# Performance work log

Measured on AMD Instinct MI355X. Metric: run time of the kernel, lower is better.

## Reference

```python
import jax, jax.numpy as jnp
import numpy as np

B, C, H, W = 8, 256, 64, 64
RED = 8
GAMMA = 1.0

def setup_inputs() -> dict:
    key = jax.random.key(0)
    k0, k1, k2, k3 = jax.random.split(key, 4)
    Cr = C // RED
    scale = 1.0 / np.sqrt(C).astype(np.float32)
    x = jax.random.normal(k0, (B, C, H, W), jnp.float32)
    # 1x1 conv weights (no bias) == channel-mixing matrices [out_c, in_c]
    w1 = jax.random.normal(k1, (Cr, C), jnp.float32) * scale  # query proj
    w2 = jax.random.normal(k2, (Cr, C), jnp.float32) * scale  # key proj
    w3 = jax.random.normal(k3, (C, C), jnp.float32) * scale   # value proj
    return {"x": x, "w1": w1, "w2": w2, "w3": w3}

def reference(x, w1, w2, w3):
    b, c, h, w = x.shape
    n = h * w
    xf = x.reshape(b, c, n)                      # [B,C,N]  (hw_flattern)
    f = jnp.einsum('oc,bcn->bon', w1, xf)        # [B,Cr,N] conv1 (1x1)
    g = jnp.einsum('oc,bcn->bon', w2, xf)        # [B,Cr,N] conv2 (1x1)
    hh = jnp.einsum('oc,bcn->bon', w3, xf)       # [B,C,N]  conv3 (1x1)
    # s = f^T g : [B,N,N]
    s = jnp.einsum('bki,bkj->bij', f, g)
    # NOTE: torch softmax over dim=1 (rows), not the usual last dim
    beta = jax.nn.softmax(s, axis=1)             # [B,N,N]
    o = jnp.einsum('bck,bkn->bcn', hh, beta)     # [B,C,N]
    o = o.reshape(b, c, h, w)
    return GAMMA * o + x
```

## Files before the change

### kernel.cpp

```cpp
#include <hip/hip_runtime.h>
#include <stdint.h>

#define Bsz 8
#define Cc  256
#define Crr 32
#define Nn  4096
#define CN  (Cc * Nn)
#define ITILE 128
#define NIT (Nn / ITILE)

typedef unsigned short u16;
typedef __attribute__((ext_vector_type(8))) short  short8;
typedef __attribute__((ext_vector_type(4))) float  floatx4;
typedef __attribute__((ext_vector_type(4))) unsigned short u16x4;

__device__ __forceinline__ floatx4 mfma16(short8 a, short8 b, floatx4 c) {
  return __builtin_amdgcn_mfma_f32_16x16x32_bf16(a, b, c, 0, 0, 0);
}
__device__ __forceinline__ u16 f2bf(float f) {
  unsigned int u = __builtin_bit_cast(unsigned int, f);
  u = (u + 0x7FFFu + ((u >> 16) & 1u)) >> 16;
  return (u16)u;
}
__device__ __forceinline__ float bf2f(u16 h) {
  unsigned int u = ((unsigned int)h) << 16;
  return __builtin_bit_cast(float, u);
}
__device__ __forceinline__ short8 pack8(const float* __restrict__ p) {
  floatx4 a = *(const floatx4*)p;
  floatx4 b = *(const floatx4*)(p + 4);
  short8 r;
  r[0] = (short)f2bf(a[0]); r[1] = (short)f2bf(a[1]);
  r[2] = (short)f2bf(a[2]); r[3] = (short)f2bf(a[3]);
  r[4] = (short)f2bf(b[0]); r[5] = (short)f2bf(b[1]);
  r[6] = (short)f2bf(b[2]); r[7] = (short)f2bf(b[3]);
  return r;
}
__device__ __forceinline__ void split8(const float* __restrict__ p,
                                       short8& hi, short8& lo) {
  floatx4 a = *(const floatx4*)p;
  floatx4 b = *(const floatx4*)(p + 4);
  float v[8] = {a[0], a[1], a[2], a[3], b[0], b[1], b[2], b[3]};
#pragma unroll
  for (int r = 0; r < 8; ++r) {
    u16 h = f2bf(v[r]);
    hi[r] = (short)h;
    lo[r] = (short)f2bf(v[r] - bf2f(h));
  }
}

template <bool XB16>
__launch_bounds__(256, 2)
__global__ void proj_kernel(const float* __restrict__ x,
                            const float* __restrict__ w1,
                            const float* __restrict__ w2,
                            const float* __restrict__ w3,
                            u16* __restrict__ w3b,
                            u16* __restrict__ fThi, u16* __restrict__ fTlo,
                            u16* __restrict__ gThi, u16* __restrict__ gTlo,
                            u16* __restrict__ xb) {
  const int bid = blockIdx.x;
  const int b   = bid & 7;
  const int nt  = bid >> 3;
  const int tid  = threadIdx.x;
  const int w    = tid >> 6;
  const int lane = tid & 63;
  const int m    = lane & 15;
  const int q    = lane >> 4;
  const int nb0  = nt * 64;
  const int nb   = nb0 + w * 16;

  __shared__ float xs[2][32 * 66];

  const float* xsl = x + (size_t)b * CN;
  const int srow = tid >> 3, scoff = (tid & 7) * 8;

  const floatx4 z4 = {0.f, 0.f, 0.f, 0.f};
  floatx4 aF[2] = {z4, z4}, aG[2] = {z4, z4};

  {
    const float* p = xsl + (size_t)(srow) * Nn + nb0 + scoff;
    floatx4 v0 = *(const floatx4*)p;
    floatx4 v1 = *(const floatx4*)(p + 4);
    float* d = &xs[0][srow * 66 + scoff];
    d[0]=v0[0]; d[1]=v0[1]; d[2]=v0[2]; d[3]=v0[3];
    d[4]=v1[0]; d[5]=v1[1]; d[6]=v1[2]; d[7]=v1[3];
  }

  for (int ci = 0; ci < 8; ++ci) {
    __syncthreads();
    if (ci + 1 < 8) {
      const float* p = xsl + (size_t)((ci + 1) * 32 + srow) * Nn + nb0 + scoff;
      floatx4 v0 = *(const floatx4*)p;
      floatx4 v1 = *(const floatx4*)(p + 4);
      float* d = &xs[(ci + 1) & 1][srow * 66 + scoff];
      d[0]=v0[0]; d[1]=v0[1]; d[2]=v0[2]; d[3]=v0[3];
      d[4]=v1[0]; d[5]=v1[1]; d[6]=v1[2]; d[7]=v1[3];
    }
    const float* xbuf = xs[ci & 1];
    const int c0 = ci * 32;
    short8 xh, xl;
#pragma unroll
    for (int r = 0; r < 8; ++r) {
      float v = xbuf[(q * 8 + r) * 66 + w * 16 + m];
      u16 h = f2bf(v);
      xh[r] = (short)h;
      xl[r] = (short)f2bf(v - bf2f(h));
    }
    if (XB16) {
      const int n  = nb + m;
      const int it = n >> 5;
      const int nq = ((n & 31) >> 3) << 4;
      const int el = n & 7;
      const size_t tb = (size_t)b * CN;
#pragma unroll
      for (int r = 0; r < 8; ++r) {
        int c = c0 + q * 8 + r;
        xb[tb + ((size_t)((it * 16 + (c >> 4)) << 9)) + ((c & 15) + nq) * 8 + el] =
            (u16)xh[r];
      }
    }
#pragma unroll
    for (int ot = 0; ot < 2; ++ot) {
      short8 wh, wl;
      split8(w1 + (size_t)(ot * 16 + m) * Cc + c0 + q * 8, wh, wl);
      aF[ot] = mfma16(xh, wh, aF[ot]);
      aF[ot] = mfma16(xh, wl, aF[ot]);
      aF[ot] = mfma16(xl, wh, aF[ot]);
      split8(w2 + (size_t)(ot * 16 + m) * Cc + c0 + q * 8, wh, wl);
      aG[ot] = mfma16(xh, wh, aG[ot]);
      aG[ot] = mfma16(xh, wl, aG[ot]);
      aG[ot] = mfma16(xl, wh, aG[ot]);
    }
  }

#pragma unroll
  for (int ot = 0; ot < 2; ++ot)
#pragma unroll
    for (int r = 0; r < 4; ++r) {
      int n = nb + q * 4 + r;
      size_t idx = ((size_t)b * Nn + n) * Crr + ot * 16 + m;
      float vf = aF[ot][r];
      u16 hf = f2bf(vf);
      fThi[idx] = hf;
      fTlo[idx] = f2bf(vf - bf2f(hf));
      float vg = aG[ot][r];
      u16 hg = f2bf(vg);
      gThi[idx] = hg;
      gTlo[idx] = f2bf(vg - bf2f(hg));
    }
  if (bid < 64) {
    int base = bid * 1024 + tid * 4;
    floatx4 v = *(const floatx4*)(w3 + base);
    u16x4 o;
    o[0] = f2bf(v[0]); o[1] = f2bf(v[1]); o[2] = f2bf(v[2]); o[3] = f2bf(v[3]);
    *(u16x4*)(w3b + base) = o;
  }
}

template <bool XB16>
__launch_bounds__(256, 2)
__global__ void attn_kernel(const u16* __restrict__ fThi,
                            const u16* __restrict__ fTlo,
                            const u16* __restrict__ gThi,
                            const u16* __restrict__ gTlo,
                            const u16* __restrict__ xb,
                            const float* __restrict__ x,
                            const u16* __restrict__ w3b,
                            float* __restrict__ out) {
  const int bid = blockIdx.x;
  const int b   = bid & 7;
  const int jt  = bid >> 3;
  const int j0  = jt * 64;
  const int tid  = threadIdx.x;
  const int w    = tid >> 6;
  const int lane = tid & 63;
  const int m    = lane & 15;
  const int q    = lane >> 4;

  __shared__ u16   P[2 * 64 * 128];
  __shared__ float lred[16 * 64];
  __shared__ float linv[64];

  const size_t fgb = (size_t)b * (size_t)Nn * Crr;
  const u16*   xbs = xb + (size_t)b * CN;
  const float* xfs = x + (size_t)b * CN;

  short8 bgh[4], bgl[4];
#pragma unroll
  for (int jb = 0; jb < 4; ++jb) {
    size_t idx = fgb + (size_t)(j0 + jb * 16 + m) * Crr + q * 8;
    bgh[jb] = *(const short8*)(gThi + idx);
    bgl[jb] = *(const short8*)(gTlo + idx);
  }

  const floatx4 z4 = {0.f, 0.f, 0.f, 0.f};
  floatx4 acc[4][4];
#pragma unroll
  for (int cb = 0; cb < 4; ++cb)
#pragma unroll
    for (int jb = 0; jb < 4; ++jb) acc[cb][jb] = z4;

  float ps[4] = {0.f, 0.f, 0.f, 0.f};
  unsigned int pw[2][4][2];
  const int iw = w * 32;
  const int cbase = w * 64;

  auto computeS = [&](int t) {
#pragma unroll
    for (int isub = 0; isub < 2; ++isub) {
      const int ig = t * ITILE + iw + isub * 16 + m;
      size_t fidx = fgb + (size_t)ig * Crr + q * 8;
      short8 afh = *(const short8*)(fThi + fidx);
      short8 afl = *(const short8*)(fTlo + fidx);
#pragma unroll
      for (int jb = 0; jb < 4; ++jb) {
        floatx4 t3 = mfma16(afl, bgh[jb], z4);
        t3 = mfma16(afh, bgl[jb], t3);
        t3 = mfma16(afh, bgh[jb], t3);
        u16 h0 = f2bf(__expf(t3[0]));
        u16 h1 = f2bf(__expf(t3[1]));
        u16 h2 = f2bf(__expf(t3[2]));
        u16 h3 = f2bf(__expf(t3[3]));
        ps[jb] += (bf2f(h0) + bf2f(h1)) + (bf2f(h2) + bf2f(h3));
        pw[isub][jb][0] = (unsigned int)h0 | ((unsigned int)h1 << 16);
        pw[isub][jb][1] = (unsigned int)h2 | ((unsigned int)h3 << 16);
      }
    }
  };

  computeS(0);

  for (int t = 0; t < NIT; ++t) {
    u16* buf = P + (t & 1) * (64 * 128);
#pragma unroll
    for (int isub = 0; isub < 2; ++isub) {
      const int g = w * 4 + isub * 2 + (q >> 1);
#pragma unroll
      for (int jb = 0; jb < 4; ++jb) {
        const int j = jb * 16 + m;
        const int ea = j * 128 + ((g ^ (j & 7)) * 8) + (q & 1) * 4;
        *(uint2*)(buf + ea) = make_uint2(pw[isub][jb][0], pw[isub][jb][1]);
      }
    }
    __syncthreads();

    if (t + 1 < NIT) computeS(t + 1);

#pragma unroll
    for (int kk = 0; kk < 4; ++kk) {
      short8 bp[4];
#pragma unroll
      for (int jb = 0; jb < 4; ++jb) {
        const int j = jb * 16 + m;
        const int g = kk * 4 + q;
        bp[jb] = *(const short8*)(buf + j * 128 + ((g ^ (j & 7)) * 8));
      }
#pragma unroll
      for (int cb = 0; cb < 4; ++cb) {
        short8 ah;
        if (XB16) {
          const int tile = (t * 4 + kk) * 16 + (w * 4 + cb);
          ah = *(const short8*)(xbs + ((size_t)tile << 9) + lane * 8);
        } else {
          ah = pack8(xfs + (size_t)(cbase + cb * 16 + m) * Nn +
                     t * ITILE + kk * 32 + q * 8);
        }
#pragma unroll
        for (int jb = 0; jb < 4; ++jb)
          acc[cb][jb] = mfma16(ah, bp[jb], acc[cb][jb]);
      }
    }
  }

#pragma unroll
  for (int jb = 0; jb < 4; ++jb)
    lred[(w * 4 + q) * 64 + jb * 16 + m] = ps[jb];
  __syncthreads();
  if (tid < 64) {
    float s = 0.f;
#pragma unroll
    for (int t = 0; t < 16; ++t) s += lred[t * 64 + tid];
    linv[tid] = 1.0f / s;
  }
  __syncthreads();

  u16* yt = P;
#pragma unroll
  for (int cb = 0; cb < 4; ++cb)
#pragma unroll
    for (int jb = 0; jb < 4; ++jb) {
      const int j = jb * 16 + m;
      const float li = linv[j];
      const int g = w * 8 + cb * 2 + (q >> 1);
      const int ea = j * 256 + ((g ^ (j & 7)) * 8) + (q & 1) * 4;
      unsigned int d0 = (unsigned int)f2bf(acc[cb][jb][0] * li) |
                        ((unsigned int)f2bf(acc[cb][jb][1] * li) << 16);
      unsigned int d1 = (unsigned int)f2bf(acc[cb][jb][2] * li) |
                        ((unsigned int)f2bf(acc[cb][jb][3] * li) << 16);
      *(uint2*)(yt + ea) = make_uint2(d0, d1);
    }
  __syncthreads();

  floatx4 macc[4][4];
#pragma unroll
  for (int ct = 0; ct < 4; ++ct)
#pragma unroll
    for (int jb = 0; jb < 4; ++jb) macc[ct][jb] = z4;

  for (int k0 = 0; k0 < Cc; k0 += 32) {
    short8 bf[4];
#pragma unroll
    for (int jb = 0; jb < 4; ++jb) {
      const int j = jb * 16 + m;
      const int g = (k0 >> 3) + q;
      bf[jb] = *(const short8*)(yt + j * 256 + ((g ^ (j & 7)) * 8));
    }
#pragma unroll
    for (int ct = 0; ct < 4; ++ct) {
      short8 aw = *(const short8*)(w3b + (size_t)(cbase + ct * 16 + m) * Cc +
                                   k0 + q * 8);
#pragma unroll
      for (int jb = 0; jb < 4; ++jb)
        macc[ct][jb] = mfma16(aw, bf[jb], macc[ct][jb]);
    }
  }

  float* osl = out + (size_t)b * CN;
#pragma unroll
  for (int ct = 0; ct < 4; ++ct)
#pragma unroll
    for (int jb = 0; jb < 4; ++jb)
#pragma unroll
      for (int r = 0; r < 4; ++r) {
        const int c = cbase + ct * 16 + q * 4 + r;
        const size_t idx = (size_t)c * Nn + j0 + jb * 16 + m;
        osl[idx] = macc[ct][jb][r] + xfs[idx];
      }
}

extern "C" void kernel_launch(void* const* d_in, const int* in_sizes, int n_in,
                              void* d_out, int out_size, void* d_ws, size_t ws_size,
                              hipStream_t stream) {
  const float* x  = (const float*)d_in[0];
  const float* w1 = (const float*)d_in[1];
  const float* w2 = (const float*)d_in[2];
  const float* w3 = (const float*)d_in[3];
  float* out = (float*)d_out;

  const size_t FG = (size_t)Bsz * Nn * Crr;
  u16* w3b  = (u16*)d_ws;
  u16* fThi = w3b + (size_t)Cc * Cc;
  u16* fTlo = fThi + FG;
  u16* gThi = fTlo + FG;
  u16* gTlo = gThi + FG;
  u16* xb   = gTlo + FG;
  const size_t need_xb = ((size_t)Cc * Cc + 4 * FG + (size_t)Bsz * CN) * 2;
  const bool use_xb = ws_size >= need_xb;

  if (use_xb) {
    proj_kernel<true><<<dim3(512), dim3(256), 0, stream>>>(
        x, w1, w2, w3, w3b, fThi, fTlo, gThi, gTlo, xb);
    attn_kernel<true><<<dim3(512), dim3(256), 0, stream>>>(
        fThi, fTlo, gThi, gTlo, xb, x, w3b, out);
  } else {
    proj_kernel<false><<<dim3(512), dim3(256), 0, stream>>>(
        x, w1, w2, w3, w3b, fThi, fTlo, gThi, gTlo, xb);
    attn_kernel<false><<<dim3(512), dim3(256), 0, stream>>>(
        fThi, fTlo, gThi, gTlo, xb, x, w3b, out);
  }
}
```

Baseline: 230.6 us.

## Split work across more waves in proj and attention kernels, use padded LDS

The projection kernel now launches twice as many blocks. It splits the channel reduction across wave pairs that combine partial sums through shared memory, and it drops the LDS staging of x in favour of direct global loads. The attention kernel moves to 512-thread blocks with 8 waves, each owning 16 rows of i and 32 channels, which halves the per-thread accumulators and raises occupancy. The XOR-swizzled LDS layouts for P and Y are replaced with padded pitches. The risks are more LDS and barrier traffic, uncoalesced strided x loads in proj, and possible bank conflicts from the new layout.

```diff
diff --git a/kernel.cpp b/kernel.cpp
--- a/kernel.cpp
+++ b/kernel.cpp
@@ -8,6 +8,8 @@
 #define CN  (Cc * Nn)
 #define ITILE 128
 #define NIT (Nn / ITILE)
+#define PPITCH 136
+#define YPITCH 264
 
 typedef unsigned short u16;
 typedef __attribute__((ext_vector_type(8))) short  short8;
@@ -50,7 +52,7 @@
 }
 
 template <bool XB16>
-__launch_bounds__(256, 2)
+__launch_bounds__(256, 4)
 __global__ void proj_kernel(const float* __restrict__ x,
                             const float* __restrict__ w1,
                             const float* __restrict__ w2,
@@ -67,42 +69,23 @@
   const int lane = tid & 63;
   const int m    = lane & 15;
   const int q    = lane >> 4;
-  const int nb0  = nt * 64;
-  const int nb   = nb0 + w * 16;
-
-  __shared__ float xs[2][32 * 66];
+  const int nhalf = w >> 1;
+  const int chalf = w & 1;
+  const int nb   = nt * 32 + nhalf * 16;
+
+  __shared__ float comb[2][16][64];
 
   const float* xsl = x + (size_t)b * CN;
-  const int srow = tid >> 3, scoff = (tid & 7) * 8;
-
   const floatx4 z4 = {0.f, 0.f, 0.f, 0.f};
   floatx4 aF[2] = {z4, z4}, aG[2] = {z4, z4};
 
-  {
-    const float* p = xsl + (size_t)(srow) * Nn + nb0 + scoff;
-    floatx4 v0 = *(const floatx4*)p;
-    floatx4 v1 = *(const floatx4*)(p + 4);
-    float* d = &xs[0][srow * 66 + scoff];
-    d[0]=v0[0]; d[1]=v0[1]; d[2]=v0[2]; d[3]=v0[3];
-    d[4]=v1[0]; d[5]=v1[1]; d[6]=v1[2]; d[7]=v1[3];
-  }
-
-  for (int ci = 0; ci < 8; ++ci) {
-    __syncthreads();
-    if (ci + 1 < 8) {
-      const float* p = xsl + (size_t)((ci + 1) * 32 + srow) * Nn + nb0 + scoff;
-      floatx4 v0 = *(const floatx4*)p;
-      floatx4 v1 = *(const floatx4*)(p + 4);
-      float* d = &xs[(ci + 1) & 1][srow * 66 + scoff];
-      d[0]=v0[0]; d[1]=v0[1]; d[2]=v0[2]; d[3]=v0[3];
-      d[4]=v1[0]; d[5]=v1[1]; d[6]=v1[2]; d[7]=v1[3];
-    }
-    const float* xbuf = xs[ci & 1];
-    const int c0 = ci * 32;
+  for (int ci = 0; ci < 4; ++ci) {
+    const int c0 = chalf * 128 + ci * 32;
+    const float* xp = xsl + (size_t)(c0 + q * 8) * Nn + nb + m;
     short8 xh, xl;
 #pragma unroll
     for (int r = 0; r < 8; ++r) {
-      float v = xbuf[(q * 8 + r) * 66 + w * 16 + m];
+      float v = xp[(size_t)r * Nn];
       u16 h = f2bf(v);
       xh[r] = (short)h;
       xl[r] = (short)f2bf(v - bf2f(h));
@@ -134,21 +117,33 @@
     }
   }
 
-#pragma unroll
-  for (int ot = 0; ot < 2; ++ot)
-#pragma unroll
-    for (int r = 0; r < 4; ++r) {
-      int n = nb + q * 4 + r;
-      size_t idx = ((size_t)b * Nn + n) * Crr + ot * 16 + m;
-      float vf = aF[ot][r];
-      u16 hf = f2bf(vf);
-      fThi[idx] = hf;
-      fTlo[idx] = f2bf(vf - bf2f(hf));
-      float vg = aG[ot][r];
-      u16 hg = f2bf(vg);
-      gThi[idx] = hg;
-      gTlo[idx] = f2bf(vg - bf2f(hg));
-    }
+  if (chalf) {
+#pragma unroll
+    for (int k = 0; k < 2; ++k)
+#pragma unroll
+      for (int r = 0; r < 4; ++r) {
+        comb[nhalf][k * 4 + r][lane]     = aF[k][r];
+        comb[nhalf][8 + k * 4 + r][lane] = aG[k][r];
+      }
+  }
+  __syncthreads();
+  if (!chalf) {
+#pragma unroll
+    for (int ot = 0; ot < 2; ++ot)
+#pragma unroll
+      for (int r = 0; r < 4; ++r) {
+        float vf = aF[ot][r] + comb[nhalf][ot * 4 + r][lane];
+        float vg = aG[ot][r] + comb[nhalf][8 + ot * 4 + r][lane];
+        int n = nb + q * 4 + r;
+        size_t idx = ((size_t)b * Nn + n) * Crr + ot * 16 + m;
+        u16 hf = f2bf(vf);
+        fThi[idx] = hf;
+        fTlo[idx] = f2bf(vf - bf2f(hf));
+        u16 hg = f2bf(vg);
+        gThi[idx] = hg;
+        gTlo[idx] = f2bf(vg - bf2f(hg));
+      }
+  }
   if (bid < 64) {
     int base = bid * 1024 + tid * 4;
     floatx4 v = *(const floatx4*)(w3 + base);
@@ -159,7 +154,7 @@
 }
 
 template <bool XB16>
-__launch_bounds__(256, 2)
+__launch_bounds__(512, 4)
 __global__ void attn_kernel(const u16* __restrict__ fThi,
                             const u16* __restrict__ fTlo,
                             const u16* __restrict__ gThi,
@@ -178,8 +173,8 @@
   const int m    = lane & 15;
   const int q    = lane >> 4;
 
-  __shared__ u16   P[2 * 64 * 128];
-  __shared__ float lred[16 * 64];
+  __shared__ u16   P[2 * 64 * PPITCH];
+  __shared__ float lred[32 * 64];
   __shared__ float linv[64];
 
   const size_t fgb = (size_t)b * (size_t)Nn * Crr;
@@ -195,53 +190,45 @@
   }
 
   const floatx4 z4 = {0.f, 0.f, 0.f, 0.f};
-  floatx4 acc[4][4];
-#pragma unroll
-  for (int cb = 0; cb < 4; ++cb)
+  floatx4 acc[2][4];
+#pragma unroll
+  for (int cb = 0; cb < 2; ++cb)
 #pragma unroll
     for (int jb = 0; jb < 4; ++jb) acc[cb][jb] = z4;
 
   float ps[4] = {0.f, 0.f, 0.f, 0.f};
-  unsigned int pw[2][4][2];
-  const int iw = w * 32;
-  const int cbase = w * 64;
+  unsigned int pw[4][2];
 
   auto computeS = [&](int t) {
-#pragma unroll
-    for (int isub = 0; isub < 2; ++isub) {
-      const int ig = t * ITILE + iw + isub * 16 + m;
-      size_t fidx = fgb + (size_t)ig * Crr + q * 8;
-      short8 afh = *(const short8*)(fThi + fidx);
-      short8 afl = *(const short8*)(fTlo + fidx);
-#pragma unroll
-      for (int jb = 0; jb < 4; ++jb) {
-        floatx4 t3 = mfma16(afl, bgh[jb], z4);
-        t3 = mfma16(afh, bgl[jb], t3);
-        t3 = mfma16(afh, bgh[jb], t3);
-        u16 h0 = f2bf(__expf(t3[0]));
-        u16 h1 = f2bf(__expf(t3[1]));
-        u16 h2 = f2bf(__expf(t3[2]));
-        u16 h3 = f2bf(__expf(t3[3]));
-        ps[jb] += (bf2f(h0) + bf2f(h1)) + (bf2f(h2) + bf2f(h3));
-        pw[isub][jb][0] = (unsigned int)h0 | ((unsigned int)h1 << 16);
-        pw[isub][jb][1] = (unsigned int)h2 | ((unsigned int)h3 << 16);
-      }
+    const int ig = t * ITILE + w * 16 + m;
+    size_t fidx = fgb + (size_t)ig * Crr + q * 8;
+    short8 afh = *(const short8*)(fThi + fidx);
+    short8 afl = *(const short8*)(fTlo + fidx);
+#pragma unroll
+    for (int jb = 0; jb < 4; ++jb) {
+      floatx4 t3 = mfma16(afl, bgh[jb], z4);
+      t3 = mfma16(afh, bgl[jb], t3);
+      t3 = mfma16(afh, bgh[jb], t3);
+      u16 h0 = f2bf(__expf(t3[0]));
+      u16 h1 = f2bf(__expf(t3[1]));
+      u16 h2 = f2bf(__expf(t3[2]));
+      u16 h3 = f2bf(__expf(t3[3]));
+      ps[jb] += (bf2f(h0) + bf2f(h1)) + (bf2f(h2) + bf2f(h3));
+      pw[jb][0] = (unsigned int)h0 | ((unsigned int)h1 << 16);
+      pw[jb][1] = (unsigned int)h2 | ((unsigned int)h3 << 16);
     }
   };
 
   computeS(0);
 
   for (int t = 0; t < NIT; ++t) {
-    u16* buf = P + (t & 1) * (64 * 128);
-#pragma unroll
-    for (int isub = 0; isub < 2; ++isub) {
-      const int g = w * 4 + isub * 2 + (q >> 1);
-#pragma unroll
-      for (int jb = 0; jb < 4; ++jb) {
-        const int j = jb * 16 + m;
-        const int ea = j * 128 + ((g ^ (j & 7)) * 8) + (q & 1) * 4;
-        *(uint2*)(buf + ea) = make_uint2(pw[isub][jb][0], pw[isub][jb][1]);
-      }
+    u16* buf = P + (t & 1) * (64 * PPITCH);
+    const int gr = w * 2 + (q >> 1);
+#pragma unroll
+    for (int jb = 0; jb < 4; ++jb) {
+      const int j = jb * 16 + m;
+      *(uint2*)(buf + j * PPITCH + gr * 8 + (q & 1) * 4) =
+          make_uint2(pw[jb][0], pw[jb][1]);
     }
     __syncthreads();
 
@@ -251,19 +238,16 @@
     for (int kk = 0; kk < 4; ++kk) {
       short8 bp[4];
 #pragma unroll
-      for (int jb = 0; jb < 4; ++jb) {
-        const int j = jb * 16 + m;
-        const int g = kk * 4 + q;
-        bp[jb] = *(const short8*)(buf + j * 128 + ((g ^ (j & 7)) * 8));
-      }
-#pragma unroll
-      for (int cb = 0; cb < 4; ++cb) {
+      for (int jb = 0; jb < 4; ++jb)
+        bp[jb] = *(const short8*)(buf + (jb * 16 + m) * PPITCH + (kk * 4 + q) * 8);
+#pragma unroll
+      for (int cb = 0; cb < 2; ++cb) {
         short8 ah;
         if (XB16) {
-          const int tile = (t * 4 + kk) * 16 + (w * 4 + cb);
+          const int tile = (t * 4 + kk) * 16 + (w * 2 + cb);
           ah = *(const short8*)(xbs + ((size_t)tile << 9) + lane * 8);
         } else {
-          ah = pack8(xfs + (size_t)(cbase + cb * 16 + m) * Nn +
+          ah = pack8(xfs + (size_t)((w * 2 + cb) * 16 + m) * Nn +
                      t * ITILE + kk * 32 + q * 8);
         }
 #pragma unroll
@@ -280,60 +264,55 @@
   if (tid < 64) {
     float s = 0.f;
 #pragma unroll
-    for (int t = 0; t < 16; ++t) s += lred[t * 64 + tid];
+    for (int t2 = 0; t2 < 32; ++t2) s += lred[t2 * 64 + tid];
     linv[tid] = 1.0f / s;
   }
   __syncthreads();
 
   u16* yt = P;
 #pragma unroll
-  for (int cb = 0; cb < 4; ++cb)
+  for (int cb = 0; cb < 2; ++cb)
 #pragma unroll
     for (int jb = 0; jb < 4; ++jb) {
       const int j = jb * 16 + m;
       const float li = linv[j];
-      const int g = w * 8 + cb * 2 + (q >> 1);
-      const int ea = j * 256 + ((g ^ (j & 7)) * 8) + (q & 1) * 4;
       unsigned int d0 = (unsigned int)f2bf(acc[cb][jb][0] * li) |
                         ((unsigned int)f2bf(acc[cb][jb][1] * li) << 16);
       unsigned int d1 = (unsigned int)f2bf(acc[cb][jb][2] * li) |
                         ((unsigned int)f2bf(acc[cb][jb][3] * li) << 16);
-      *(uint2*)(yt + ea) = make_uint2(d0, d1);
+      *(uint2*)(yt + j * YPITCH + (w * 2 + cb) * 16 + q * 4) = make_uint2(d0, d1);
     }
   __syncthreads();
 
-  floatx4 macc[4][4];
-#pragma unroll
-  for (int ct = 0; ct < 4; ++ct)
+  floatx4 macc[2][4];
+#pragma unroll
+  for (int ct = 0; ct < 2; ++ct)
 #pragma unroll
     for (int jb = 0; jb < 4; ++jb) macc[ct][jb] = z4;
 
   for (int k0 = 0; k0 < Cc; k0 += 32) {
-    short8 bf[4];
-#pragma unroll
-    for (int jb = 0; jb < 4; ++jb) {
-      const int j = jb * 16 + m;
-      const int g = (k0 >> 3) + q;
-      bf[jb] = *(const short8*)(yt + j * 256 + ((g ^ (j & 7)) * 8));
-    }
-#pragma unroll
-    for (int ct = 0; ct < 4; ++ct) {
-      short8 aw = *(const short8*)(w3b + (size_t)(cbase + ct * 16 + m) * Cc +
+    short8 bf_[4];
+#pragma unroll
+    for (int jb = 0; jb < 4; ++jb)
+      bf_[jb] = *(const short8*)(yt + (jb * 16 + m) * YPITCH + k0 + q * 8);
+#pragma unroll
+    for (int ct = 0; ct < 2; ++ct) {
+      short8 aw = *(const short8*)(w3b + (size_t)((w * 2 + ct) * 16 + m) * Cc +
                                    k0 + q * 8);
 #pragma unroll
       for (int jb = 0; jb < 4; ++jb)
-        macc[ct][jb] = mfma16(aw, bf[jb], macc[ct][jb]);
+        macc[ct][jb] = mfma16(aw, bf_[jb], macc[ct][jb]);
     }
   }
 
   float* osl = out + (size_t)b * CN;
 #pragma unroll
-  for (int ct = 0; ct < 4; ++ct)
+  for (int ct = 0; ct < 2; ++ct)
 #pragma unroll
     for (int jb = 0; jb < 4; ++jb)
 #pragma unroll
       for (int r = 0; r < 4; ++r) {
-        const int c = cbase + ct * 16 + q * 4 + r;
+        const int c = (w * 2 + ct) * 16 + q * 4 + r;
         const size_t idx = (size_t)c * Nn + j0 + jb * 16 + m;
         osl[idx] = macc[ct][jb][r] + xfs[idx];
       }
@@ -359,14 +338,14 @@
   const bool use_xb = ws_size >= need_xb;
 
   if (use_xb) {
-    proj_kernel<true><<<dim3(512), dim3(256), 0, stream>>>(
+    proj_kernel<true><<<dim3(1024), dim3(256), 0, stream>>>(
         x, w1, w2, w3, w3b, fThi, fTlo, gThi, gTlo, xb);
-    attn_kernel<true><<<dim3(512), dim3(256), 0, stream>>>(
+    attn_kernel<true><<<dim3(512), dim3(512), 0, stream>>>(
         fThi, fTlo, gThi, gTlo, xb, x, w3b, out);
   } else {
-    proj_kernel<false><<<dim3(512), dim3(256), 0, stream>>>(
+    proj_kernel<false><<<dim3(1024), dim3(256), 0, stream>>>(
         x, w1, w2, w3, w3b, fThi, fTlo, gThi, gTlo, xb);
-    attn_kernel<false><<<dim3(512), dim3(256), 0, stream>>>(
+    attn_kernel<false><<<dim3(512), dim3(512), 0, stream>>>(
         fThi, fTlo, gThi, gTlo, xb, x, w3b, out);
   }
 }
```

Measured after the change: 234.6 us. No clear change (+1.7%).
